# Performance work log

Measured on AMD Instinct MI355X. Metric: run time of the kernel, lower is better.

Reference implementation:

```python
import jax, jax.numpy as jnp
import numpy as np

WINDOW = (7, 7)
SHIFT = (3, 3)
NUM_HEADS = 4
DIM = 128


def _rel_pos_index():
    wh, ww = WINDOW
    coords = np.stack(np.meshgrid(np.arange(wh), np.arange(ww), indexing='ij'))  # [2,wh,ww]
    cf = coords.reshape(2, -1)                    # [2, N]
    rc = (cf[:, :, None] - cf[:, None, :]).transpose(1, 2, 0)  # [N,N,2]
    rc[:, :, 0] += wh - 1
    rc[:, :, 1] += ww - 1
    rc[:, :, 0] *= 2 * ww - 1
    return jnp.asarray(rc.sum(-1).reshape(-1))    # [N*N] int


def _attn_mask_np(pH, pW, sh):
    # Static-shape shift mask (host-side numpy; constant under jit).
    wh, ww = WINDOW
    m = np.zeros((pH, pW))
    h_slices = ((0, pH - wh), (pH - wh, pH - sh[0]), (pH - sh[0], pH))
    w_slices = ((0, pW - ww), (pW - ww, pW - sh[1]), (pW - sh[1], pW))
    cnt = 0
    for hs in h_slices:
        for ws in w_slices:
            m[hs[0]:hs[1], ws[0]:ws[1]] = cnt
            cnt += 1
    m = m.reshape(pH // wh, wh, pW // ww, ww).transpose(0, 2, 1, 3).reshape(-1, wh * ww)
    diff = m[:, None, :] - m[:, :, None]          # [num_windows, N, N]
    return jnp.asarray(np.where(diff != 0, -100.0, 0.0), dtype=np.float32)


def setup_inputs() -> dict:
    key = jax.random.key(0)
    ks = jax.random.split(key, 9)
    B, H, W, C = 32, 56, 56, DIM
    return {
        'input_q': jax.random.normal(ks[0], (B, H, W, C), jnp.float32),
        'input_k': jax.random.normal(ks[1], (B, H, W, C), jnp.float32),
        'input_v': jax.random.normal(ks[2], (B, H, W, C), jnp.float32),
        'q_weight': jax.random.normal(ks[3], (C, C), jnp.float32) * 0.05,
        'q_bias': jnp.zeros((C,), jnp.float32),
        'k_weight': jax.random.normal(ks[4], (C, C), jnp.float32) * 0.05,
        'k_bias': jnp.zeros((C,), jnp.float32),
        'v_weight': jax.random.normal(ks[5], (C, C), jnp.float32) * 0.05,
        'v_bias': jnp.zeros((C,), jnp.float32),
        'proj_weight': jax.random.normal(ks[6], (C, C), jnp.float32) * 0.05,
        'proj_bias': jnp.zeros((C,), jnp.float32),
        'rpb_table': jax.random.normal(ks[7], ((2 * WINDOW[0] - 1) * (2 * WINDOW[1] - 1), NUM_HEADS), jnp.float32) * 0.02,
    }


def reference(input_q, input_k, input_v, q_weight, q_bias, k_weight, k_bias,
              v_weight, v_bias, proj_weight, proj_bias, rpb_table):
    B, H, W, C = input_q.shape
    wh, ww = WINDOW
    pad_b = (wh - H % wh) % wh
    pad_r = (ww - W % ww) % ww
    pad = lambda t: jnp.pad(t, ((0, 0), (0, pad_b), (0, pad_r), (0, 0)))
    qx, kx, vx = pad(input_q), pad(input_k), pad(input_v)
    pad_H, pad_W = H + pad_b, W + pad_r
    sh = [0 if wh >= pad_H else SHIFT[0], 0 if ww >= pad_W else SHIFT[1]]
    if sum(sh) > 0:
        roll = lambda t: jnp.roll(t, (-sh[0], -sh[1]), axis=(1, 2))
        qx, kx, vx = roll(qx), roll(kx), roll(vx)
    nWh, nWw = pad_H // wh, pad_W // ww
    num_windows = nWh * nWw
    N = wh * ww

    def part(t):  # [B,pH,pW,C] -> [B*num_windows, N, C]
        t = t.reshape(B, nWh, wh, nWw, ww, C).transpose(0, 1, 3, 2, 4, 5)
        return t.reshape(B * num_windows, N, C)

    qx, kx, vx = part(qx), part(kx), part(vx)
    hd = C // NUM_HEADS

    def heads(x, w, b):  # linear + split heads -> [BW, nH, N, hd]
        return (x @ w.T + b).reshape(-1, N, NUM_HEADS, hd).transpose(0, 2, 1, 3)

    q = heads(qx, q_weight, q_bias) * (hd ** -0.5)
    k = heads(kx, k_weight, k_bias)
    v = heads(vx, v_weight, v_bias)

    attn = jnp.einsum('whqd,whkd->whqk', q, k)    # [BW, nH, N, N]
    rpb = rpb_table[_rel_pos_index()].reshape(N, N, NUM_HEADS).transpose(2, 0, 1)[None]
    attn = attn + rpb
    if sum(sh) > 0:
        mask = _attn_mask_np(pad_H, pad_W, sh)    # [num_windows, N, N]
        attn = attn.reshape(B, num_windows, NUM_HEADS, N, N) + mask[None, :, None]
        attn = attn.reshape(B * num_windows, NUM_HEADS, N, N)
    attn = jax.nn.softmax(attn, axis=-1)

    x = jnp.einsum('whqk,whkd->whqd', attn, v).transpose(0, 2, 1, 3).reshape(B * num_windows, N, C)
    x = x @ proj_weight.T + proj_bias
    x = x.reshape(B, nWh, nWw, wh, ww, C).transpose(0, 1, 3, 2, 4, 5).reshape(B, pad_H, pad_W, C)
    if sum(sh) > 0:
        x = jnp.roll(x, (sh[0], sh[1]), axis=(1, 2))
    return x[:, :H, :W, :]
```

## Files before the change

### kernel.cpp

```cpp
#include <hip/hip_runtime.h>
#include <hip/hip_bf16.h>

typedef __attribute__((ext_vector_type(8))) short s16x8;
typedef __attribute__((ext_vector_type(4))) float f32x4;
typedef __attribute__((ext_vector_type(2))) unsigned int u32x2;
typedef __attribute__((ext_vector_type(4))) unsigned int u32x4;

#define MFMA16(a, b, c) __builtin_amdgcn_mfma_f32_16x16x32_bf16((a), (b), (c), 0, 0, 0)
#define LOG2E 1.4426950408889634f

static __device__ __forceinline__ unsigned int pk2(float a, float b) {
  union { __hip_bfloat162 h2; unsigned int u; } cv;
  cv.h2 = __float22bfloat162_rn(make_float2(a, b));
  return cv.u;
}
static __device__ __forceinline__ int div7(int x) { return (x * 9363) >> 16; }
static __device__ __forceinline__ int swz256(int row, int byteoff) {
  return row * 256 + (byteoff ^ ((row & 7) << 4));
}
static __device__ __forceinline__ int swz128(int row, int byteoff) {
  return row * 128 + (byteoff ^ ((row & 7) << 4));
}

__global__ void swin_prep(const float* __restrict__ wq, const float* __restrict__ wk,
                          const float* __restrict__ wv, const float* __restrict__ wp,
                          const float* __restrict__ rpb_table,
                          unsigned short* __restrict__ wsW, float* __restrict__ rpbm) {
  int idx = blockIdx.x * 256 + threadIdx.x;
  if (idx < 65536) {
    int t = idx >> 14, loc = idx & 16383;
    const float* s = (t == 0) ? wq : (t == 1) ? wk : (t == 2) ? wv : wp;
    union { __hip_bfloat16 h; unsigned short u; } cv;
    cv.h = __float2bfloat16(s[loc]);
    wsW[idx] = cv.u;
  } else {
    int k = idx - 65536;
    int c = k >> 14;
    int h = (k >> 12) & 3;
    int i = (k >> 6) & 63, j = k & 63;
    float val;
    if (j >= 49) val = -1e30f;
    else if (i >= 49) val = 0.f;
    else {
      int yi = div7(i), xi = i - yi * 7;
      int yj = div7(j), xj = j - yj * 7;
      int ridx = (yi - yj + 6) * 13 + (xi - xj + 6);
      val = rpb_table[ridx * 4 + h];
      int cwi = c >> 1, cwj = c & 1;
      int rgi = (cwi ? (yi < 4 ? 3 : 6) : 0) + (cwj ? (xi < 4 ? 1 : 2) : 0);
      int rgj = (cwi ? (yj < 4 ? 3 : 6) : 0) + (cwj ? (xj < 4 ? 1 : 2) : 0);
      if (rgi != rgj) val -= 100.f;
      val *= LOG2E;
    }
    rpbm[k] = val;
  }
}

__global__ __launch_bounds__(512, 4) void swin_main(
    const float* __restrict__ xq, const float* __restrict__ xk, const float* __restrict__ xv,
    const float* __restrict__ bq, const float* __restrict__ bk, const float* __restrict__ bv,
    const float* __restrict__ bp, const unsigned short* __restrict__ wsW,
    const float* __restrict__ rpbm, float* __restrict__ out) {
  __shared__ __align__(16) char sm[65536];

  const int tid = threadIdx.x;
  const int lane = tid & 63;
  const int wv_ = tid >> 6;
  const int l15 = lane & 15;
  const int lg = lane >> 4;
  const int kgrp = lg * 8;
  const int rsub = lg * 4;

  const int bid = blockIdx.x;
  const int b = bid >> 6;
  const int widx = bid & 63;
  const int wi = widx >> 3, wj = widx & 7;
  const long obase = (long)b * 56 * 56 * 128;
  const int mcase = ((wi == 7) ? 2 : 0) + ((wj == 7) ? 1 : 0);

  const int h = wv_ & 3;
  const int half = wv_ >> 2;
  const int coff = h * 32;

  f32x4 rvv[2][4];
  {
    const float* rpbm_h = rpbm + (((mcase << 2) + h) << 12);
#pragma unroll
    for (int m2 = 0; m2 < 2; ++m2)
#pragma unroll
      for (int r = 0; r < 4; ++r) {
        int i = (half * 2 + m2) * 16 + rsub + r;
        const float* rp = rpbm_h + i * 64 + l15;
#pragma unroll
        for (int jt = 0; jt < 4; ++jt) rvv[m2][jt][r] = rp[jt * 16];
      }
  }

  const int xrow = tid >> 3;
  const int xk16 = (tid & 7) << 4;
  long xoff = -1;
  if (xrow < 49) {
    int ty = div7(xrow), tx = xrow - ty * 7;
    int ih = wi * 7 + ty + 3; if (ih >= 56) ih -= 56;
    int iw = wj * 7 + tx + 3; if (iw >= 56) iw -= 56;
    xoff = obase + (long)((ih * 56 + iw) * 128 + xk16);
  }

  auto issue_x = [&](const float* src, float* r) {
#pragma unroll
    for (int i = 0; i < 16; ++i) r[i] = 0.f;
    if (xoff >= 0) {
      const float* p = src + xoff;
#pragma unroll
      for (int q = 0; q < 4; ++q) {
        f32x4 v = *(const f32x4*)(p + q * 4);
        r[q * 4 + 0] = v[0]; r[q * 4 + 1] = v[1];
        r[q * 4 + 2] = v[2]; r[q * 4 + 3] = v[3];
      }
    }
  };
  auto write_x = [&](int base, const float* r) {
    unsigned int w[8];
#pragma unroll
    for (int i = 0; i < 8; ++i) w[i] = pk2(r[2 * i], r[2 * i + 1]);
    u32x4 a = {w[0], w[1], w[2], w[3]};
    u32x4 bb = {w[4], w[5], w[6], w[7]};
    *(u32x4*)(sm + base + swz256(xrow, xk16 * 2)) = a;
    *(u32x4*)(sm + base + swz256(xrow, xk16 * 2 + 16)) = bb;
  };
  auto st2 = [&](int a0, int a1, float v0, float v1) {
    unsigned int u = pk2(v0, v1);
    *(unsigned short*)(sm + a0) = (unsigned short)u;
    *(unsigned short*)(sm + a1) = (unsigned short)(u >> 16);
  };

  auto linearT = [&](int woff, const float* bias, float scale, int srcbase, int dstbase) {
    const int nrow = wv_ * 16 + l15;
    s16x8 afr[4];
#pragma unroll
    for (int kt = 0; kt < 4; ++kt)
      afr[kt] = *(const s16x8*)(wsW + woff + nrow * 128 + kt * 32 + kgrp);
    f32x4 bv4 = *(const f32x4*)(bias + wv_ * 16 + rsub);
    float bb0 = bv4[0] * scale, bb1 = bv4[1] * scale;
    float bb2 = bv4[2] * scale, bb3 = bv4[3] * scale;
#pragma unroll
    for (int tt = 0; tt < 4; ++tt) {
      f32x4 acc = {0.f, 0.f, 0.f, 0.f};
#pragma unroll
      for (int kt = 0; kt < 4; ++kt) {
        s16x8 bfr = *(const s16x8*)(sm + srcbase + swz256(tt * 16 + l15, (kt * 32 + kgrp) * 2));
        acc = MFMA16(afr[kt], bfr, acc);
      }
      u32x2 pkw = {pk2(acc[0] * scale + bb0, acc[1] * scale + bb1),
                   pk2(acc[2] * scale + bb2, acc[3] * scale + bb3)};
      *(u32x2*)(sm + dstbase + swz256(tt * 16 + l15, 2 * (wv_ * 16 + rsub))) = pkw;
    }
  };

  auto linearV = [&](int woff, const float* bias) {
    const int n = wv_ * 16 + l15;
    s16x8 bfr[4];
#pragma unroll
    for (int kt = 0; kt < 4; ++kt)
      bfr[kt] = *(const s16x8*)(wsW + woff + n * 128 + kt * 32 + kgrp);
    float bval = bias[n];
#pragma unroll
    for (int mt = 0; mt < 4; ++mt) {
      f32x4 acc = {0.f, 0.f, 0.f, 0.f};
#pragma unroll
      for (int kt = 0; kt < 4; ++kt) {
        s16x8 afr = *(const s16x8*)(sm + swz256(mt * 16 + l15, (kt * 32 + kgrp) * 2));
        acc = MFMA16(afr, bfr[kt], acc);
      }
      u32x2 pkw = {pk2(acc[0] + bval, acc[1] + bval), pk2(acc[2] + bval, acc[3] + bval)};
      *(u32x2*)(sm + 49152 + swz128(n, 2 * (mt * 16 + rsub))) = pkw;
    }
  };

  const float QSCALE = 0.17677669529663687f * LOG2E;

  float xra[16], xrb[16];
  issue_x(xq, xra);
  issue_x(xk, xrb);
  write_x(0, xra);
  write_x(49152, xrb);
  __syncthreads();

  issue_x(xv, xra);
  linearT(0, bq, QSCALE, 0, 16384);
  __syncthreads();

  write_x(0, xra);
  linearT(16384, bk, 1.f, 49152, 32768);
  __syncthreads();

  f32x4 S[2][4];
  {
    linearV(32768, bv);

    s16x8 kfr[4];
#pragma unroll
    for (int jt = 0; jt < 4; ++jt)
      kfr[jt] = *(const s16x8*)(sm + 32768 + swz256(jt * 16 + l15, (coff + kgrp) * 2));
    __builtin_amdgcn_s_setprio(1);
#pragma unroll
    for (int m2 = 0; m2 < 2; ++m2) {
      int mt = half * 2 + m2;
      s16x8 qfr = *(const s16x8*)(sm + 16384 + swz256(mt * 16 + l15, (coff + kgrp) * 2));
#pragma unroll
      for (int jt = 0; jt < 4; ++jt)
        S[m2][jt] = MFMA16(qfr, kfr[jt], rvv[m2][jt]);
    }
    __builtin_amdgcn_s_setprio(0);

#pragma unroll
    for (int m2 = 0; m2 < 2; ++m2) {
#pragma unroll
      for (int r = 0; r < 4; ++r) {
        float m = fmaxf(fmaxf(S[m2][0][r], S[m2][1][r]), fmaxf(S[m2][2][r], S[m2][3][r]));
        for (int d = 1; d < 16; d <<= 1) m = fmaxf(m, __shfl_xor(m, d));
        float e0 = exp2f(S[m2][0][r] - m);
        float e1 = exp2f(S[m2][1][r] - m);
        float e2 = exp2f(S[m2][2][r] - m);
        float e3 = exp2f(S[m2][3][r] - m);
        float s = e0 + e1 + e2 + e3;
        for (int d = 1; d < 16; d <<= 1) s += __shfl_xor(s, d);
        float inv = 1.0f / s;
        S[m2][0][r] = e0 * inv; S[m2][1][r] = e1 * inv;
        S[m2][2][r] = e2 * inv; S[m2][3][r] = e3 * inv;
      }
    }
  }
  __syncthreads();

  const int pbase = 16384 + h * 8192;
#pragma unroll
  for (int m2 = 0; m2 < 2; ++m2) {
    int i0 = (half * 2 + m2) * 16 + rsub;
#pragma unroll
    for (int jt = 0; jt < 4; ++jt) {
      int bo = 2 * (jt * 16 + l15);
      st2(pbase + swz128(i0, bo), pbase + swz128(i0 + 1, bo), S[m2][jt][0], S[m2][jt][1]);
      st2(pbase + swz128(i0 + 2, bo), pbase + swz128(i0 + 3, bo), S[m2][jt][2], S[m2][jt][3]);
    }
  }
  {
    s16x8 vfr[2][2];
#pragma unroll
    for (int ks = 0; ks < 2; ++ks)
#pragma unroll
      for (int ct = 0; ct < 2; ++ct) {
        int c = coff + ct * 16 + l15;
        vfr[ks][ct] = *(const s16x8*)(sm + 49152 + swz128(c, (ks * 32 + kgrp) * 2));
      }
    f32x4 Oacc[2][2];
#pragma unroll
    for (int ct = 0; ct < 2; ++ct)
#pragma unroll
      for (int qt = 0; qt < 2; ++qt) Oacc[ct][qt] = (f32x4){0.f, 0.f, 0.f, 0.f};
    __builtin_amdgcn_s_setprio(1);
#pragma unroll
    for (int qt = 0; qt < 2; ++qt) {
#pragma unroll
      for (int ks = 0; ks < 2; ++ks) {
        s16x8 pfr = *(const s16x8*)(sm + pbase + swz128((half * 2 + qt) * 16 + l15, (ks * 32 + kgrp) * 2));
        Oacc[0][qt] = MFMA16(vfr[ks][0], pfr, Oacc[0][qt]);
        Oacc[1][qt] = MFMA16(vfr[ks][1], pfr, Oacc[1][qt]);
      }
    }
    __builtin_amdgcn_s_setprio(0);
#pragma unroll
    for (int ct = 0; ct < 2; ++ct)
#pragma unroll
      for (int qt = 0; qt < 2; ++qt) {
        int qtok = (half * 2 + qt) * 16 + l15;
        u32x2 pkw = {pk2(Oacc[ct][qt][0], Oacc[ct][qt][1]),
                     pk2(Oacc[ct][qt][2], Oacc[ct][qt][3])};
        *(u32x2*)(sm + swz256(qtok, 2 * (coff + ct * 16 + rsub))) = pkw;
      }
  }
  __syncthreads();

  {
    const int nrow = wv_ * 16 + l15;
    s16x8 afr[4];
#pragma unroll
    for (int kt = 0; kt < 4; ++kt)
      afr[kt] = *(const s16x8*)(wsW + 49152 + nrow * 128 + kt * 32 + kgrp);
    f32x4 bv4 = *(const f32x4*)(bp + wv_ * 16 + rsub);
#pragma unroll
    for (int tt = 0; tt < 4; ++tt) {
      f32x4 acc = {0.f, 0.f, 0.f, 0.f};
#pragma unroll
      for (int kt = 0; kt < 4; ++kt) {
        s16x8 bfr = *(const s16x8*)(sm + swz256(tt * 16 + l15, (kt * 32 + kgrp) * 2));
        acc = MFMA16(afr[kt], bfr, acc);
      }
      int tok = tt * 16 + l15;
      if (tok < 49) {
        int ty = div7(tok), tx = tok - ty * 7;
        int oh = wi * 7 + ty + 3; if (oh >= 56) oh -= 56;
        int ow = wj * 7 + tx + 3; if (ow >= 56) ow -= 56;
        f32x4 res = {acc[0] + bv4[0], acc[1] + bv4[1], acc[2] + bv4[2], acc[3] + bv4[3]};
        *(f32x4*)(out + obase + (oh * 56 + ow) * 128 + wv_ * 16 + rsub) = res;
      }
    }
  }
}

extern "C" void kernel_launch(void* const* d_in, const int* in_sizes, int n_in,
                              void* d_out, int out_size, void* d_ws, size_t ws_size,
                              hipStream_t stream) {
  const float* xq = (const float*)d_in[0];
  const float* xk = (const float*)d_in[1];
  const float* xv = (const float*)d_in[2];
  const float* wq = (const float*)d_in[3];
  const float* bq = (const float*)d_in[4];
  const float* wk = (const float*)d_in[5];
  const float* bk = (const float*)d_in[6];
  const float* wv = (const float*)d_in[7];
  const float* bv = (const float*)d_in[8];
  const float* wp = (const float*)d_in[9];
  const float* bp = (const float*)d_in[10];
  const float* rpb = (const float*)d_in[11];

  unsigned short* wsW = (unsigned short*)d_ws;
  float* rpbm = (float*)((char*)d_ws + 131072);

  swin_prep<<<512, 256, 0, stream>>>(wq, wk, wv, wp, rpb, wsW, rpbm);

  float* out = (float*)d_out;
  swin_main<<<2048, 512, 0, stream>>>(xq, xk, xv, bq, bk, bv, bp, wsW, rpbm, out);
}
```

Before: 78.50 us.

## Keep softmax probabilities in registers and feed PV MFMA via lane shuffles

The QK^T MFMA operands are swapped so each lane holds a query row's scores along the register axis. This lets softmax reduce mostly in-lane with only two cross-lane shuffles. The normalized probabilities are packed to bf16 in registers and rearranged with xor-shuffles into the B-operand layout of the PV MFMA, removing the LDS store and reload of the P matrix. Other changes: input and bias prefetch loads are hoisted earlier, the bias loads are vectorized, raw exp2 is used, and MFMA sections in the linear layers get raised priority. The cost is extra shuffle and select instructions, plus a transposed bias-table layout assumption.

```diff
diff --git a/kernel.cpp b/kernel.cpp
--- a/kernel.cpp
+++ b/kernel.cpp
@@ -82,20 +82,6 @@
   const int half = wv_ >> 2;
   const int coff = h * 32;
 
-  f32x4 rvv[2][4];
-  {
-    const float* rpbm_h = rpbm + (((mcase << 2) + h) << 12);
-#pragma unroll
-    for (int m2 = 0; m2 < 2; ++m2)
-#pragma unroll
-      for (int r = 0; r < 4; ++r) {
-        int i = (half * 2 + m2) * 16 + rsub + r;
-        const float* rp = rpbm_h + i * 64 + l15;
-#pragma unroll
-        for (int jt = 0; jt < 4; ++jt) rvv[m2][jt][r] = rp[jt * 16];
-      }
-  }
-
   const int xrow = tid >> 3;
   const int xk16 = (tid & 7) << 4;
   long xoff = -1;
@@ -128,11 +114,22 @@
     *(u32x4*)(sm + base + swz256(xrow, xk16 * 2)) = a;
     *(u32x4*)(sm + base + swz256(xrow, xk16 * 2 + 16)) = bb;
   };
-  auto st2 = [&](int a0, int a1, float v0, float v1) {
-    unsigned int u = pk2(v0, v1);
-    *(unsigned short*)(sm + a0) = (unsigned short)u;
-    *(unsigned short*)(sm + a1) = (unsigned short)(u >> 16);
-  };
+
+  float xra[16], xrb[16];
+  issue_x(xq, xra);
+  issue_x(xk, xrb);
+
+  f32x4 rvv[2][4];
+  {
+    const float* rpbm_h = rpbm + (((mcase << 2) + h) << 12);
+#pragma unroll
+    for (int m2 = 0; m2 < 2; ++m2) {
+      const float* rp = rpbm_h + ((half * 2 + m2) * 16 + l15) * 64 + rsub;
+#pragma unroll
+      for (int jt = 0; jt < 4; ++jt)
+        rvv[m2][jt] = *(const f32x4*)(rp + jt * 16);
+    }
+  }
 
   auto linearT = [&](int woff, const float* bias, float scale, int srcbase, int dstbase) {
     const int nrow = wv_ * 16 + l15;
@@ -143,6 +140,7 @@
     f32x4 bv4 = *(const f32x4*)(bias + wv_ * 16 + rsub);
     float bb0 = bv4[0] * scale, bb1 = bv4[1] * scale;
     float bb2 = bv4[2] * scale, bb3 = bv4[3] * scale;
+    __builtin_amdgcn_s_setprio(1);
 #pragma unroll
     for (int tt = 0; tt < 4; ++tt) {
       f32x4 acc = {0.f, 0.f, 0.f, 0.f};
@@ -155,6 +153,7 @@
                    pk2(acc[2] * scale + bb2, acc[3] * scale + bb3)};
       *(u32x2*)(sm + dstbase + swz256(tt * 16 + l15, 2 * (wv_ * 16 + rsub))) = pkw;
     }
+    __builtin_amdgcn_s_setprio(0);
   };
 
   auto linearV = [&](int woff, const float* bias) {
@@ -164,6 +163,7 @@
     for (int kt = 0; kt < 4; ++kt)
       bfr[kt] = *(const s16x8*)(wsW + woff + n * 128 + kt * 32 + kgrp);
     float bval = bias[n];
+    __builtin_amdgcn_s_setprio(1);
 #pragma unroll
     for (int mt = 0; mt < 4; ++mt) {
       f32x4 acc = {0.f, 0.f, 0.f, 0.f};
@@ -175,13 +175,11 @@
       u32x2 pkw = {pk2(acc[0] + bval, acc[1] + bval), pk2(acc[2] + bval, acc[3] + bval)};
       *(u32x2*)(sm + 49152 + swz128(n, 2 * (mt * 16 + rsub))) = pkw;
     }
+    __builtin_amdgcn_s_setprio(0);
   };
 
   const float QSCALE = 0.17677669529663687f * LOG2E;
 
-  float xra[16], xrb[16];
-  issue_x(xq, xra);
-  issue_x(xk, xrb);
   write_x(0, xra);
   write_x(49152, xrb);
   __syncthreads();
@@ -194,7 +192,7 @@
   linearT(16384, bk, 1.f, 49152, 32768);
   __syncthreads();
 
-  f32x4 S[2][4];
+  unsigned int pw[2][4][2];
   {
     linearV(32768, bv);
 
@@ -202,6 +200,7 @@
 #pragma unroll
     for (int jt = 0; jt < 4; ++jt)
       kfr[jt] = *(const s16x8*)(sm + 32768 + swz256(jt * 16 + l15, (coff + kgrp) * 2));
+    f32x4 S[2][4];
     __builtin_amdgcn_s_setprio(1);
 #pragma unroll
     for (int m2 = 0; m2 < 2; ++m2) {
@@ -209,41 +208,40 @@
       s16x8 qfr = *(const s16x8*)(sm + 16384 + swz256(mt * 16 + l15, (coff + kgrp) * 2));
 #pragma unroll
       for (int jt = 0; jt < 4; ++jt)
-        S[m2][jt] = MFMA16(qfr, kfr[jt], rvv[m2][jt]);
+        S[m2][jt] = MFMA16(kfr[jt], qfr, rvv[m2][jt]);
     }
     __builtin_amdgcn_s_setprio(0);
 
 #pragma unroll
     for (int m2 = 0; m2 < 2; ++m2) {
-#pragma unroll
-      for (int r = 0; r < 4; ++r) {
-        float m = fmaxf(fmaxf(S[m2][0][r], S[m2][1][r]), fmaxf(S[m2][2][r], S[m2][3][r]));
-        for (int d = 1; d < 16; d <<= 1) m = fmaxf(m, __shfl_xor(m, d));
-        float e0 = exp2f(S[m2][0][r] - m);
-        float e1 = exp2f(S[m2][1][r] - m);
-        float e2 = exp2f(S[m2][2][r] - m);
-        float e3 = exp2f(S[m2][3][r] - m);
-        float s = e0 + e1 + e2 + e3;
-        for (int d = 1; d < 16; d <<= 1) s += __shfl_xor(s, d);
-        float inv = 1.0f / s;
-        S[m2][0][r] = e0 * inv; S[m2][1][r] = e1 * inv;
-        S[m2][2][r] = e2 * inv; S[m2][3][r] = e3 * inv;
-      }
-    }
-  }
-  __syncthreads();
-
-  const int pbase = 16384 + h * 8192;
-#pragma unroll
-  for (int m2 = 0; m2 < 2; ++m2) {
-    int i0 = (half * 2 + m2) * 16 + rsub;
-#pragma unroll
-    for (int jt = 0; jt < 4; ++jt) {
-      int bo = 2 * (jt * 16 + l15);
-      st2(pbase + swz128(i0, bo), pbase + swz128(i0 + 1, bo), S[m2][jt][0], S[m2][jt][1]);
-      st2(pbase + swz128(i0 + 2, bo), pbase + swz128(i0 + 3, bo), S[m2][jt][2], S[m2][jt][3]);
-    }
-  }
+      float m = S[m2][0][0];
+#pragma unroll
+      for (int jt = 0; jt < 4; ++jt)
+#pragma unroll
+        for (int r = 0; r < 4; ++r) m = fmaxf(m, S[m2][jt][r]);
+      m = fmaxf(m, __shfl_xor(m, 16));
+      m = fmaxf(m, __shfl_xor(m, 32));
+      float sum = 0.f;
+#pragma unroll
+      for (int jt = 0; jt < 4; ++jt)
+#pragma unroll
+        for (int r = 0; r < 4; ++r) {
+          float e = __builtin_amdgcn_exp2f(S[m2][jt][r] - m);
+          S[m2][jt][r] = e;
+          sum += e;
+        }
+      sum += __shfl_xor(sum, 16);
+      sum += __shfl_xor(sum, 32);
+      float inv = 1.0f / sum;
+#pragma unroll
+      for (int jt = 0; jt < 4; ++jt) {
+        pw[m2][jt][0] = pk2(S[m2][jt][0] * inv, S[m2][jt][1] * inv);
+        pw[m2][jt][1] = pk2(S[m2][jt][2] * inv, S[m2][jt][3] * inv);
+      }
+    }
+  }
+  __syncthreads();
+
   {
     s16x8 vfr[2][2];
 #pragma unroll
@@ -258,17 +256,28 @@
     for (int ct = 0; ct < 2; ++ct)
 #pragma unroll
       for (int qt = 0; qt < 2; ++qt) Oacc[ct][qt] = (f32x4){0.f, 0.f, 0.f, 0.f};
-    __builtin_amdgcn_s_setprio(1);
 #pragma unroll
     for (int qt = 0; qt < 2; ++qt) {
 #pragma unroll
       for (int ks = 0; ks < 2; ++ks) {
-        s16x8 pfr = *(const s16x8*)(sm + pbase + swz128((half * 2 + qt) * 16 + l15, (ks * 32 + kgrp) * 2));
-        Oacc[0][qt] = MFMA16(vfr[ks][0], pfr, Oacc[0][qt]);
-        Oacc[1][qt] = MFMA16(vfr[ks][1], pfr, Oacc[1][qt]);
-      }
-    }
-    __builtin_amdgcn_s_setprio(0);
+        unsigned int lo[2], hi[2];
+#pragma unroll
+        for (int g = 0; g < 2; ++g) {
+          unsigned int p0 = pw[qt][2 * ks][g], p1 = pw[qt][2 * ks + 1][g];
+          unsigned int r16 = __shfl_xor((lg & 2) ? p1 : p0, 16);
+          unsigned int r32 = __shfl_xor((lg & 2) ? p0 : p1, 32);
+          unsigned int r48 = __shfl_xor((lg & 1) ? p1 : p0, 48);
+          lo[g] = (lg == 0) ? p0 : (lg == 1) ? r48 : (lg == 2) ? r32 : r16;
+          hi[g] = (lg == 0) ? r16 : (lg == 1) ? r32 : (lg == 2) ? r48 : p1;
+        }
+        union { u32x4 u; s16x8 s; } pf;
+        pf.u = (u32x4){lo[0], lo[1], hi[0], hi[1]};
+        __builtin_amdgcn_s_setprio(1);
+        Oacc[0][qt] = MFMA16(vfr[ks][0], pf.s, Oacc[0][qt]);
+        Oacc[1][qt] = MFMA16(vfr[ks][1], pf.s, Oacc[1][qt]);
+        __builtin_amdgcn_s_setprio(0);
+      }
+    }
 #pragma unroll
     for (int ct = 0; ct < 2; ++ct)
 #pragma unroll
@@ -288,6 +297,7 @@
     for (int kt = 0; kt < 4; ++kt)
       afr[kt] = *(const s16x8*)(wsW + 49152 + nrow * 128 + kt * 32 + kgrp);
     f32x4 bv4 = *(const f32x4*)(bp + wv_ * 16 + rsub);
+    __builtin_amdgcn_s_setprio(1);
 #pragma unroll
     for (int tt = 0; tt < 4; ++tt) {
       f32x4 acc = {0.f, 0.f, 0.f, 0.f};
@@ -305,6 +315,7 @@
         *(f32x4*)(out + obase + (oh * 56 + ow) * 128 + wv_ * 16 + rsub) = res;
       }
     }
+    __builtin_amdgcn_s_setprio(0);
   }
 }
 
```

Result: slower. 80.99 us (+3.2%).
